# Optimization experiments

Hardware: AMD Instinct MI355X
Metric: run time of the kernel (lower is better)

Reference implementation:

```python
import jax, jax.numpy as jnp
import numpy as np
from jax import lax

V, D, B, S = 50000, 300, 32, 128
H = 1024          # LSTM hidden per direction
NT = 9            # number of CRF tags
BN_EPS = 1e-5


def setup_inputs() -> dict:
    key = jax.random.key(0)
    ks = iter(jax.random.split(key, 48))
    def nrm(shape, scale=0.05):
        return jax.random.normal(next(ks), shape, dtype=jnp.float32) * scale
    inp = {}
    inp["x"] = jax.random.randint(next(ks), (B, S), 0, V)
    inp["y"] = jax.random.randint(next(ks), (B, S), 0, NT)
    inp["mask"] = jnp.ones((B, S), dtype=bool)
    inp["emb"] = nrm((V, D), 0.1)
    inp["lin1_w"] = nrm((512, D)); inp["lin1_b"] = jnp.zeros((512,), jnp.float32)
    in_sizes = [512, 2 * H, 2 * H, 2 * H]
    for l, isz in enumerate(in_sizes):
        inp[f"wih{l}"] = nrm((2, 4 * H, isz))   # [dir, 4H, in]
        inp[f"whh{l}"] = nrm((2, 4 * H, H))
        inp[f"bias{l}"] = jnp.zeros((2, 4 * H), jnp.float32)  # b_ih + b_hh combined
    inp["bn_gamma"] = jnp.ones((2 * H,), jnp.float32)
    inp["bn_beta"] = jnp.zeros((2 * H,), jnp.float32)
    inp["lin2_w"] = nrm((NT, 2 * H)); inp["lin2_b"] = jnp.zeros((NT,), jnp.float32)
    inp["crf_start"] = nrm((NT,), 0.1)
    inp["crf_end"] = nrm((NT,), 0.1)
    inp["crf_trans"] = nrm((NT, NT), 0.1)
    return inp


def _lstm_dir(xs, Wih, Whh, b):
    # xs: [S, B, in] -> hs: [S, B, H]; torch gate order i, f, g, o
    pre = jnp.einsum('sbi,gi->sbg', xs, Wih) + b  # [S,B,4H]
    h0 = jnp.zeros((xs.shape[1], Whh.shape[1]), xs.dtype)
    def step(carry, p):
        h, c = carry
        g = p + h @ Whh.T
        i, f, gg, o = jnp.split(g, 4, axis=-1)
        c = jax.nn.sigmoid(f) * c + jax.nn.sigmoid(i) * jnp.tanh(gg)
        h = jax.nn.sigmoid(o) * jnp.tanh(c)
        return (h, c), h
    _, hs = lax.scan(step, (h0, h0), pre)
    return hs


def _bilstm(xs, Wih, Whh, b):
    fwd = _lstm_dir(xs, Wih[0], Whh[0], b[0])
    bwd = _lstm_dir(xs[::-1], Wih[1], Whh[1], b[1])[::-1]
    return jnp.concatenate([fwd, bwd], axis=-1)


def _crf_llh(emis, tags, mask, start, end, trans):
    # torchcrf CRF forward, batch_first, reduction='sum'
    mf = mask.astype(emis.dtype)
    e_tag = jnp.take_along_axis(emis, tags[..., None], -1)[..., 0]  # [B,S]
    num = start[tags[:, 0]] + e_tag[:, 0]
    tr = trans[tags[:, :-1], tags[:, 1:]]                           # [B,S-1]
    num = num + jnp.sum(mf[:, 1:] * (tr + e_tag[:, 1:]), axis=1)
    lengths = mask.sum(axis=1).astype(jnp.int32)
    last_tag = jnp.take_along_axis(tags, (lengths - 1)[:, None], 1)[:, 0]
    num = num + end[last_tag]
    # forward algorithm (log-sum-exp recurrence over seq)
    alpha0 = start + emis[:, 0]                                     # [B,NT]
    seq_e = jnp.transpose(emis[:, 1:], (1, 0, 2))                   # [S-1,B,NT]
    seq_m = jnp.transpose(mask[:, 1:], (1, 0))                      # [S-1,B]
    def step(alpha, inp):
        e_t, m_t = inp
        nxt = jax.nn.logsumexp(alpha[:, :, None] + trans[None] + e_t[:, None, :], axis=1)
        return jnp.where(m_t[:, None], nxt, alpha), None
    alpha, _ = lax.scan(step, alpha0, (seq_e, seq_m))
    den = jax.nn.logsumexp(alpha + end, axis=1)
    return jnp.sum(num - den)


def reference(x, y, mask, emb, lin1_w, lin1_b,
              wih0, whh0, bias0, wih1, whh1, bias1,
              wih2, whh2, bias2, wih3, whh3, bias3,
              bn_gamma, bn_beta, lin2_w, lin2_b,
              crf_start, crf_end, crf_trans):
    h = emb[x]                          # [B,S,D]
    h = h @ lin1_w.T + lin1_b           # [B,S,512]
    hs = jnp.transpose(h, (1, 0, 2))    # [S,B,512]
    for Wih, Whh, bb in ((wih0, whh0, bias0), (wih1, whh1, bias1),
                         (wih2, whh2, bias2), (wih3, whh3, bias3)):
        hs = _bilstm(hs, Wih, Whh, bb)  # [S,B,2048]
    h = jnp.transpose(hs, (1, 0, 2))    # [B,S,2048]
    # BatchNorm1d eval (running mean 0, var 1) -> affine; ReLU; Dropout eval = id
    h = jax.nn.relu(bn_gamma * h / jnp.sqrt(jnp.float32(1.0 + BN_EPS)) + bn_beta)
    emis = h @ lin2_w.T + lin2_b        # [B,S,9]
    return _crf_llh(emis, y, mask, crf_start, crf_end, crf_trans)
```

## Files before the change

### kernel.cpp

```cpp
#include <hip/hip_runtime.h>
#include <hip/hip_bf16.h>

typedef __attribute__((ext_vector_type(8))) short short8;
typedef __attribute__((ext_vector_type(4))) float f32x4;
typedef unsigned short ushort_t;
typedef unsigned long long u64_t;

__device__ __forceinline__ ushort_t f2bf(float f) {
    __hip_bfloat16 h = __float2bfloat16(f);
    return *(ushort_t*)&h;
}
__device__ __forceinline__ float bf2f(ushort_t u) {
    union { float f; unsigned u32; } x; x.u32 = ((unsigned)u) << 16; return x.f;
}
__device__ __forceinline__ float sigmoidf_(float x) { return 1.0f / (1.0f + expf(-x)); }

__device__ __forceinline__ short8 cvt8(const float* p) {
    short8 r;
    #pragma unroll
    for (int j = 0; j < 8; j++) r[j] = (short)f2bf(p[j]);
    return r;
}

__global__ void lin1_pad(const float* __restrict__ w, ushort_t* __restrict__ d) {
    int idx = blockIdx.x * 256 + threadIdx.x;
    if (idx >= 512 * 320) return;
    int n = idx / 320, k = idx % 320;
    d[idx] = (k < 300) ? f2bf(w[n * 300 + k]) : (ushort_t)0;
}

__global__ void wcvt(const float* __restrict__ w, ushort_t* __restrict__ d, int n) {
    int idx = (blockIdx.x * 256 + threadIdx.x) * 8;
    if (idx >= n) return;
    float tmp[8];
    *(float4*)&tmp[0] = *(const float4*)(w + idx);
    *(float4*)&tmp[4] = *(const float4*)(w + idx + 4);
    *(short8*)&d[idx] = cvt8(tmp);
}

__global__ void emb_gather(const int* __restrict__ x, const float* __restrict__ emb,
                           ushort_t* __restrict__ XE) {
    int tok = blockIdx.x;
    int s = tok >> 5, b = tok & 31;
    int row = x[b * 128 + s];
    const float* e = emb + (size_t)row * 300;
    for (int d = threadIdx.x; d < 320; d += 64)
        XE[(size_t)tok * 320 + d] = (d < 300) ? f2bf(e[d]) : (ushort_t)0;
}

template<bool WF32, bool F32OUT>
__global__ __launch_bounds__(256) void gemm_bias(
    const ushort_t* __restrict__ X, const void* __restrict__ Wv,
    const float* __restrict__ bias, void* __restrict__ Cv,
    int K, int ldx, int ldw, int ldc)
{
    __shared__ __align__(16) ushort_t As[4 * 64 * 8];
    __shared__ __align__(16) ushort_t Bs[4 * 64 * 8];
    const int tid = threadIdx.x;
    const int lane = tid & 63;
    const int w = tid >> 6;
    const int wm = w & 1, wn = w >> 1;
    const int m0 = blockIdx.x * 64, n0 = blockIdx.y * 64;
    const int mt = tid >> 6;
    const int r = lane & 15, q = lane >> 4;
    const ushort_t* xsrc = X + (size_t)(m0 + mt * 16 + r) * ldx + q * 8;
    const ushort_t* wsrcb = WF32 ? nullptr : (const ushort_t*)Wv + (size_t)(n0 + mt * 16 + r) * ldw + q * 8;
    const float*    wsrcf = WF32 ? (const float*)Wv + (size_t)(n0 + mt * 16 + r) * ldw + q * 8 : nullptr;
    f32x4 acc00 = {0,0,0,0}, acc01 = {0,0,0,0}, acc10 = {0,0,0,0}, acc11 = {0,0,0,0};
    for (int k0 = 0; k0 < K; k0 += 32) {
        __syncthreads();
        *(uint4*)&As[(mt * 64 + lane) * 8] = *(const uint4*)(xsrc + k0);
        if (WF32) {
            float tmp[8];
            *(float4*)&tmp[0] = *(const float4*)(wsrcf + k0);
            *(float4*)&tmp[4] = *(const float4*)(wsrcf + k0 + 4);
            *(short8*)&Bs[(mt * 64 + lane) * 8] = cvt8(tmp);
        } else {
            *(uint4*)&Bs[(mt * 64 + lane) * 8] = *(const uint4*)(wsrcb + k0);
        }
        __syncthreads();
        short8 a0 = *(const short8*)&As[((2 * wm    ) * 64 + lane) * 8];
        short8 a1 = *(const short8*)&As[((2 * wm + 1) * 64 + lane) * 8];
        short8 b0 = *(const short8*)&Bs[((2 * wn    ) * 64 + lane) * 8];
        short8 b1 = *(const short8*)&Bs[((2 * wn + 1) * 64 + lane) * 8];
        acc00 = __builtin_amdgcn_mfma_f32_16x16x32_bf16(a0, b0, acc00, 0, 0, 0);
        acc01 = __builtin_amdgcn_mfma_f32_16x16x32_bf16(a0, b1, acc01, 0, 0, 0);
        acc10 = __builtin_amdgcn_mfma_f32_16x16x32_bf16(a1, b0, acc10, 0, 0, 0);
        acc11 = __builtin_amdgcn_mfma_f32_16x16x32_bf16(a1, b1, acc11, 0, 0, 0);
    }
    const int mb = m0 + wm * 32, nb = n0 + wn * 32;
    f32x4 accs[2][2] = {{acc00, acc01}, {acc10, acc11}};
    for (int i = 0; i < 2; i++)
        for (int j = 0; j < 2; j++) {
            int n = nb + j * 16 + r;
            float bv = bias[n];
            #pragma unroll
            for (int reg = 0; reg < 4; reg++) {
                int m = mb + i * 16 + q * 4 + reg;
                float v = accs[i][j][reg] + bv;
                if (F32OUT) ((float*)Cv)[(size_t)m * ldc + n] = v;
                else ((ushort_t*)Cv)[(size_t)m * ldc + n] = f2bf(v);
            }
        }
}

__device__ __forceinline__ void gbar(unsigned* flags, int dir, int slice, int epoch) {
    __syncthreads();
    if (threadIdx.x == 0)
        __hip_atomic_store(&flags[(dir * 32 + slice) * 16], (unsigned)epoch,
                           __ATOMIC_RELAXED, __HIP_MEMORY_SCOPE_AGENT);
    if (threadIdx.x < 64) {
        const unsigned* f = &flags[(dir * 32 + (threadIdx.x & 31)) * 16];
        int spins = 0;
        while (true) {
            unsigned v = __hip_atomic_load(f, __ATOMIC_RELAXED, __HIP_MEMORY_SCOPE_AGENT);
            if (__all(v >= (unsigned)epoch)) break;
            __builtin_amdgcn_s_sleep(1);
            if (++spins >= 65536) {
                spins = 0;
                v = __hip_atomic_load(f, __ATOMIC_ACQUIRE, __HIP_MEMORY_SCOPE_AGENT);
                if (__all(v >= (unsigned)epoch)) break;
            }
        }
    }
    __syncthreads();
}

__global__ __launch_bounds__(512) void lstm_scan(
    const float* __restrict__ PRE,
    const float* __restrict__ WHH,
    ushort_t* __restrict__ H,
    ushort_t* __restrict__ OUT,
    unsigned* __restrict__ flags,
    int epoch0)
{
    const int tid = threadIdx.x;
    const int lane = tid & 63;
    const int w = tid >> 6;
    const int dir = blockIdx.x >> 5;
    const int slice = blockIdx.x & 31;
    const int u0 = slice * 32;
    __shared__ __align__(16) ushort_t Af[2 * 32 * 64 * 8];
    __shared__ float gl[32 * 132];

    const int colw = w * 16 + (lane & 15);
    short8 bfr[32];
    {
        const int gate = colw >> 5, unit = colw & 31;
        const float* wrow = WHH + ((size_t)(dir * 4096 + gate * 1024 + u0 + unit)) * 1024 + (lane >> 4) * 8;
        #pragma unroll
        for (int kc = 0; kc < 32; kc++) {
            float tmp[8];
            *(float4*)&tmp[0] = *(const float4*)(wrow + kc * 32);
            *(float4*)&tmp[4] = *(const float4*)(wrow + kc * 32 + 4);
            bfr[kc] = cvt8(tmp);
        }
    }
    const int eb = tid >> 4, eu = tid & 15;
    float cst0 = 0.f, cst1 = 0.f;
    if ((eu & 1) == 0) {
        ushort_t* hz = H + (size_t)((0 * 2 + dir) * 32 + eb) * 1024 + u0;
        __hip_atomic_store((unsigned*)(hz + eu),      0u, __ATOMIC_RELAXED, __HIP_MEMORY_SCOPE_AGENT);
        __hip_atomic_store((unsigned*)(hz + 16 + eu), 0u, __ATOMIC_RELAXED, __HIP_MEMORY_SCOPE_AGENT);
    }
    int epoch = epoch0 + 1;
    gbar(flags, dir, slice, epoch);

    for (int t = 0; t < 128; t++) {
        const int s = dir ? (127 - t) : t;
        const int bufr = t & 1, bufw = bufr ^ 1;
        const ushort_t* Hsrc = H + (size_t)((bufr * 2 + dir) * 32) * 1024;
        u64_t tmp[16];
        #pragma unroll
        for (int i = 0; i < 8; i++) {
            int c = tid + i * 512;
            int ln = c & 63;
            int kc = (c >> 6) & 31;
            int mt2 = c >> 11;
            int b = mt2 * 16 + (ln & 15);
            int k = kc * 32 + (ln >> 4) * 8;
            const u64_t* src = (const u64_t*)(Hsrc + (size_t)b * 1024 + k);
            tmp[2 * i]     = __hip_atomic_load(src,     __ATOMIC_RELAXED, __HIP_MEMORY_SCOPE_AGENT);
            tmp[2 * i + 1] = __hip_atomic_load(src + 1, __ATOMIC_RELAXED, __HIP_MEMORY_SCOPE_AGENT);
        }
        float pb[8];
        {
            const float* pp = PRE + ((size_t)(s * 32 + eb)) * 8192 + (size_t)dir * 4096 + u0 + eu;
            #pragma unroll
            for (int g = 0; g < 4; g++) {
                pb[2 * g]     = pp[g * 1024];
                pb[2 * g + 1] = pp[g * 1024 + 16];
            }
        }
        #pragma unroll
        for (int i = 0; i < 8; i++) {
            int c = tid + i * 512;
            *(u64_t*)&Af[(size_t)c * 8]     = tmp[2 * i];
            *(u64_t*)&Af[(size_t)c * 8 + 4] = tmp[2 * i + 1];
        }
        __syncthreads();
        f32x4 acc0 = {0,0,0,0}, acc1 = {0,0,0,0};
        #pragma unroll
        for (int kc = 0; kc < 32; kc++) {
            short8 a0 = *(const short8*)&Af[(size_t)((     kc) * 64 + lane) * 8];
            short8 a1 = *(const short8*)&Af[(size_t)((32 + kc) * 64 + lane) * 8];
            acc0 = __builtin_amdgcn_mfma_f32_16x16x32_bf16(a0, bfr[kc], acc0, 0, 0, 0);
            acc1 = __builtin_amdgcn_mfma_f32_16x16x32_bf16(a1, bfr[kc], acc1, 0, 0, 0);
        }
        const int rowb = (lane >> 4) * 4;
        #pragma unroll
        for (int reg = 0; reg < 4; reg++) {
            gl[(rowb + reg) * 132 + colw]        = acc0[reg];
            gl[(16 + rowb + reg) * 132 + colw]   = acc1[reg];
        }
        __syncthreads();
        {
            float gi0 = gl[eb * 132 +  0 + eu] + pb[0];
            float gi1 = gl[eb * 132 + 16 + eu] + pb[1];
            float gf0 = gl[eb * 132 + 32 + eu] + pb[2];
            float gf1 = gl[eb * 132 + 48 + eu] + pb[3];
            float gg0 = gl[eb * 132 + 64 + eu] + pb[4];
            float gg1 = gl[eb * 132 + 80 + eu] + pb[5];
            float go0 = gl[eb * 132 + 96 + eu] + pb[6];
            float go1 = gl[eb * 132 + 112 + eu] + pb[7];
            cst0 = sigmoidf_(gf0) * cst0 + sigmoidf_(gi0) * tanhf(gg0);
            cst1 = sigmoidf_(gf1) * cst1 + sigmoidf_(gi1) * tanhf(gg1);
            float h0 = sigmoidf_(go0) * tanhf(cst0);
            float h1 = sigmoidf_(go1) * tanhf(cst1);
            ushort_t hb0 = f2bf(h0), hb1 = f2bf(h1);
            unsigned o0 = (unsigned)(ushort_t)__shfl_xor((int)(unsigned)hb0, 1);
            unsigned o1 = (unsigned)(ushort_t)__shfl_xor((int)(unsigned)hb1, 1);
            if ((eu & 1) == 0) {
                ushort_t* hw = H + (size_t)((bufw * 2 + dir) * 32 + eb) * 1024 + u0;
                __hip_atomic_store((unsigned*)(hw + eu),      (unsigned)hb0 | (o0 << 16),
                                   __ATOMIC_RELAXED, __HIP_MEMORY_SCOPE_AGENT);
                __hip_atomic_store((unsigned*)(hw + 16 + eu), (unsigned)hb1 | (o1 << 16),
                                   __ATOMIC_RELAXED, __HIP_MEMORY_SCOPE_AGENT);
            }
            ushort_t* op = OUT + ((size_t)(s * 32 + eb)) * 2048 + (size_t)dir * 1024 + u0;
            op[eu] = hb0;
            op[16 + eu] = hb1;
        }
        epoch++;
        gbar(flags, dir, slice, epoch);
    }
}

__global__ __launch_bounds__(256) void emis_kernel(
    const ushort_t* __restrict__ Xf,
    const float* __restrict__ gamma, const float* __restrict__ beta,
    const float* __restrict__ w2, const float* __restrict__ b2,
    float* __restrict__ EM)
{
    const int lane = threadIdx.x & 63;
    const int wv = threadIdx.x >> 6;
    const int tok = blockIdx.x * 4 + wv;
    const int s = tok >> 5, b = tok & 31;
    const float inv = 0.9999950000374997f;
    const int j0 = lane * 4;
    float hn[32];
    #pragma unroll
    for (int c = 0; c < 8; c++) {
        int j = j0 + c * 256;
        u64_t xv = *(const u64_t*)(Xf + (size_t)tok * 2048 + j);
        float4 gv = *(const float4*)(gamma + j);
        float4 bv = *(const float4*)(beta + j);
        float x0 = bf2f((ushort_t)(xv      )), x1 = bf2f((ushort_t)(xv >> 16));
        float x2 = bf2f((ushort_t)(xv >> 32)), x3 = bf2f((ushort_t)(xv >> 48));
        float h0 = gv.x * x0 * inv + bv.x;
        float h1 = gv.y * x1 * inv + bv.y;
        float h2 = gv.z * x2 * inv + bv.z;
        float h3 = gv.w * x3 * inv + bv.w;
        hn[c * 4 + 0] = h0 > 0.f ? h0 : 0.f;
        hn[c * 4 + 1] = h1 > 0.f ? h1 : 0.f;
        hn[c * 4 + 2] = h2 > 0.f ? h2 : 0.f;
        hn[c * 4 + 3] = h3 > 0.f ? h3 : 0.f;
    }
    float acc[9];
    #pragma unroll
    for (int k = 0; k < 9; k++) {
        const float* wr = w2 + (size_t)k * 2048 + j0;
        float a = 0.f;
        #pragma unroll
        for (int c = 0; c < 8; c++) {
            float4 wv4 = *(const float4*)(wr + c * 256);
            a += hn[c * 4 + 0] * wv4.x + hn[c * 4 + 1] * wv4.y
               + hn[c * 4 + 2] * wv4.z + hn[c * 4 + 3] * wv4.w;
        }
        acc[k] = a;
    }
    #pragma unroll
    for (int k = 0; k < 9; k++) {
        #pragma unroll
        for (int off = 32; off > 0; off >>= 1)
            acc[k] += __shfl_xor(acc[k], off);
    }
    if (lane == 0) {
        float* em = EM + ((size_t)b * 128 + s) * 9;
        #pragma unroll
        for (int k = 0; k < 9; k++) em[k] = acc[k] + b2[k];
    }
}

__global__ __launch_bounds__(512) void crf_kernel(
    const float* __restrict__ EM,
    const int* __restrict__ y,
    const float* __restrict__ start, const float* __restrict__ endw,
    const float* __restrict__ trans,
    float* __restrict__ out)
{
    __shared__ float tr[81], st[9], en[9];
    __shared__ float alpha[2][32][12];
    __shared__ float numsh[32], densh[32];
    int tid = threadIdx.x;
    if (tid < 81) tr[tid] = trans[tid];
    if (tid < 9) { st[tid] = start[tid]; en[tid] = endw[tid]; }
    __syncthreads();
    if (tid < 32) {
        int b = tid;
        const int* yb = y + b * 128;
        const float* ebm = EM + (size_t)b * 1152;
        float num = st[yb[0]] + ebm[yb[0]];
        for (int s = 1; s < 128; s++)
            num += tr[yb[s - 1] * 9 + yb[s]] + ebm[s * 9 + yb[s]];
        num += en[yb[127]];
        numsh[b] = num;
    }
    int b = tid / 9, k = tid % 9;
    bool act = tid < 288;
    if (act) alpha[0][b][k] = st[k] + EM[(size_t)b * 1152 + k];
    __syncthreads();
    for (int s = 1; s < 128; s++) {
        int cur = s & 1, prv = cur ^ 1;
        if (act) {
            float m = -1e30f;
            #pragma unroll
            for (int j = 0; j < 9; j++)
                m = fmaxf(m, alpha[prv][b][j] + tr[j * 9 + k]);
            float sum = 0.f;
            #pragma unroll
            for (int j = 0; j < 9; j++)
                sum += expf(alpha[prv][b][j] + tr[j * 9 + k] - m);
            alpha[cur][b][k] = m + logf(sum) + EM[(size_t)b * 1152 + s * 9 + k];
        }
        __syncthreads();
    }
    if (tid < 32) {
        float m = -1e30f;
        for (int j = 0; j < 9; j++) m = fmaxf(m, alpha[1][tid][j] + en[j]);
        float sum = 0.f;
        for (int j = 0; j < 9; j++) sum += expf(alpha[1][tid][j] + en[j] - m);
        densh[tid] = m + logf(sum);
    }
    __syncthreads();
    if (tid == 0) {
        float tot = 0.f;
        for (int bb = 0; bb < 32; bb++) tot += numsh[bb] - densh[bb];
        out[0] = tot;
    }
}

extern "C" void kernel_launch(void* const* d_in, const int* in_sizes, int n_in,
                              void* d_out, int out_size, void* d_ws, size_t ws_size,
                              hipStream_t stream) {
    const int*   x       = (const int*)d_in[0];
    const int*   y       = (const int*)d_in[1];
    const float* emb     = (const float*)d_in[3];
    const float* lin1_w  = (const float*)d_in[4];
    const float* lin1_b  = (const float*)d_in[5];
    const float* wih[4]  = {(const float*)d_in[6],  (const float*)d_in[9],
                            (const float*)d_in[12], (const float*)d_in[15]};
    const float* whh[4]  = {(const float*)d_in[7],  (const float*)d_in[10],
                            (const float*)d_in[13], (const float*)d_in[16]};
    const float* biasl[4]= {(const float*)d_in[8],  (const float*)d_in[11],
                            (const float*)d_in[14], (const float*)d_in[17]};
    const float* bn_g    = (const float*)d_in[18];
    const float* bn_b    = (const float*)d_in[19];
    const float* lin2_w  = (const float*)d_in[20];
    const float* lin2_b  = (const float*)d_in[21];
    const float* crf_s   = (const float*)d_in[22];
    const float* crf_e   = (const float*)d_in[23];
    const float* crf_t   = (const float*)d_in[24];

    char* ws = (char*)d_ws;
    size_t off = 0;
    auto alloc = [&](size_t bytes) { size_t r = off; off += (bytes + 255) & ~(size_t)255; return r; };
    size_t oFLG  = alloc(4096);
    size_t oXE   = alloc((size_t)4096 * 320 * 2);
    size_t oWL1  = alloc((size_t)512 * 320 * 2);
    size_t oXB0  = alloc((size_t)4096 * 2048 * 2);
    size_t oXB1  = alloc((size_t)4096 * 2048 * 2);
    size_t oPRE  = alloc((size_t)4096 * 8192 * 4);
    size_t oH    = alloc((size_t)2 * 2 * 32 * 1024 * 2);
    size_t oEM   = alloc((size_t)32 * 128 * 9 * 4);
    size_t oWB   = alloc((size_t)8192 * 2048 * 2);
    (void)ws_size; (void)in_sizes; (void)n_in; (void)out_size;

    unsigned* flags = (unsigned*)(ws + oFLG);
    ushort_t* XE   = (ushort_t*)(ws + oXE);
    ushort_t* WL1  = (ushort_t*)(ws + oWL1);
    ushort_t* XB0  = (ushort_t*)(ws + oXB0);
    ushort_t* XB1  = (ushort_t*)(ws + oXB1);
    float*    PRE  = (float*)(ws + oPRE);
    ushort_t* Hb   = (ushort_t*)(ws + oH);
    float*    EM   = (float*)(ws + oEM);
    ushort_t* WB   = (ushort_t*)(ws + oWB);

    hipMemsetAsync(ws + oFLG, 0, 4096, stream);
    emb_gather<<<4096, 64, 0, stream>>>(x, emb, XE);
    lin1_pad<<<(512 * 320 + 255) / 256, 256, 0, stream>>>(lin1_w, WL1);
    gemm_bias<false, false><<<dim3(64, 8), 256, 0, stream>>>(XE, WL1, lin1_b, XB0, 320, 320, 320, 512);

    for (int l = 0; l < 4; l++) {
        int Kl = (l == 0) ? 512 : 2048;
        ushort_t* Xin  = (l % 2 == 0) ? XB0 : XB1;
        ushort_t* Xout = (l % 2 == 0) ? XB1 : XB0;
        int nw = 8192 * Kl;
        wcvt<<<nw / 2048, 256, 0, stream>>>(wih[l], WB, nw);
        gemm_bias<false, true><<<dim3(64, 128), 256, 0, stream>>>(Xin, WB, biasl[l], PRE,
                                                                  Kl, Kl, Kl, 8192);
        lstm_scan<<<64, 512, 0, stream>>>(PRE, whh[l], Hb, Xout, flags, l * 129);
    }
    emis_kernel<<<1024, 256, 0, stream>>>(XB0, bn_g, bn_b, lin2_w, lin2_b, EM);
    crf_kernel<<<1, 512, 0, stream>>>(EM, y, crf_s, crf_e, crf_t, (float*)d_out);
}
```

Baseline: 5.726 ms.

## Permute input-projection output per slice and prefetch next step's gate inputs

The input-projection GEMM now writes its fp32 output in a layout ordered by direction, slice and timestep, with each thread's two units held next to each other, so the LSTM scan can read its eight gate pre-activations as four float2 loads from one contiguous region. The scan also issues the loads for step t+1 during step t, taking global-memory latency off the serial recurrence. In exchange, the GEMM epilogue does scattered stores and needs more address arithmetic, and the scan holds a few extra registers.

New measurement: 5.682 ms. No clear change (-0.8%).

```diff
diff --git a/kernel.cpp b/kernel.cpp
--- a/kernel.cpp
+++ b/kernel.cpp
@@ -48,7 +48,7 @@
         XE[(size_t)tok * 320 + d] = (d < 300) ? f2bf(e[d]) : (ushort_t)0;
 }
 
-template<bool WF32, bool F32OUT>
+template<bool WF32, bool F32OUT, bool PERM>
 __global__ __launch_bounds__(256) void gemm_bias(
     const ushort_t* __restrict__ X, const void* __restrict__ Wv,
     const float* __restrict__ bias, void* __restrict__ Cv,
@@ -94,12 +94,26 @@
         for (int j = 0; j < 2; j++) {
             int n = nb + j * 16 + r;
             float bv = bias[n];
-            #pragma unroll
-            for (int reg = 0; reg < 4; reg++) {
-                int m = mb + i * 16 + q * 4 + reg;
-                float v = accs[i][j][reg] + bv;
-                if (F32OUT) ((float*)Cv)[(size_t)m * ldc + n] = v;
-                else ((ushort_t*)Cv)[(size_t)m * ldc + n] = f2bf(v);
+            if (PERM) {
+                int dirn = n >> 12, c = n & 4095;
+                int gate = c >> 10, unit = c & 1023;
+                int slice = unit >> 5, ue5 = unit & 31;
+                int pos = ((ue5 & 15) << 1) | (ue5 >> 4);
+                float* base = (float*)Cv + ((size_t)(dirn * 32 + slice) * 128) * 4096 + gate * 32 + pos;
+                #pragma unroll
+                for (int reg = 0; reg < 4; reg++) {
+                    int m = mb + i * 16 + q * 4 + reg;
+                    int ss = m >> 5, bb = m & 31;
+                    base[(size_t)ss * 4096 + bb * 128] = accs[i][j][reg] + bv;
+                }
+            } else {
+                #pragma unroll
+                for (int reg = 0; reg < 4; reg++) {
+                    int m = mb + i * 16 + q * 4 + reg;
+                    float v = accs[i][j][reg] + bv;
+                    if (F32OUT) ((float*)Cv)[(size_t)m * ldc + n] = v;
+                    else ((ushort_t*)Cv)[(size_t)m * ldc + n] = f2bf(v);
+                }
             }
         }
 }
@@ -163,6 +177,15 @@
         __hip_atomic_store((unsigned*)(hz + eu),      0u, __ATOMIC_RELAXED, __HIP_MEMORY_SCOPE_AGENT);
         __hip_atomic_store((unsigned*)(hz + 16 + eu), 0u, __ATOMIC_RELAXED, __HIP_MEMORY_SCOPE_AGENT);
     }
+    const float* pbase = PRE + ((size_t)(dir * 32 + slice) * 128) * 4096 + eb * 128 + (eu << 1);
+    float2 pb0, pb1, pb2, pb3;
+    {
+        const float* pp = pbase + (size_t)(dir ? 127 : 0) * 4096;
+        pb0 = *(const float2*)(pp);
+        pb1 = *(const float2*)(pp + 32);
+        pb2 = *(const float2*)(pp + 64);
+        pb3 = *(const float2*)(pp + 96);
+    }
     int epoch = epoch0 + 1;
     gbar(flags, dir, slice, epoch);
 
@@ -183,15 +206,6 @@
             tmp[2 * i]     = __hip_atomic_load(src,     __ATOMIC_RELAXED, __HIP_MEMORY_SCOPE_AGENT);
             tmp[2 * i + 1] = __hip_atomic_load(src + 1, __ATOMIC_RELAXED, __HIP_MEMORY_SCOPE_AGENT);
         }
-        float pb[8];
-        {
-            const float* pp = PRE + ((size_t)(s * 32 + eb)) * 8192 + (size_t)dir * 4096 + u0 + eu;
-            #pragma unroll
-            for (int g = 0; g < 4; g++) {
-                pb[2 * g]     = pp[g * 1024];
-                pb[2 * g + 1] = pp[g * 1024 + 16];
-            }
-        }
         #pragma unroll
         for (int i = 0; i < 8; i++) {
             int c = tid + i * 512;
@@ -215,14 +229,21 @@
         }
         __syncthreads();
         {
-            float gi0 = gl[eb * 132 +  0 + eu] + pb[0];
-            float gi1 = gl[eb * 132 + 16 + eu] + pb[1];
-            float gf0 = gl[eb * 132 + 32 + eu] + pb[2];
-            float gf1 = gl[eb * 132 + 48 + eu] + pb[3];
-            float gg0 = gl[eb * 132 + 64 + eu] + pb[4];
-            float gg1 = gl[eb * 132 + 80 + eu] + pb[5];
-            float go0 = gl[eb * 132 + 96 + eu] + pb[6];
-            float go1 = gl[eb * 132 + 112 + eu] + pb[7];
+            float gi0 = gl[eb * 132 +   0 + eu] + pb0.x;
+            float gi1 = gl[eb * 132 +  16 + eu] + pb0.y;
+            float gf0 = gl[eb * 132 +  32 + eu] + pb1.x;
+            float gf1 = gl[eb * 132 +  48 + eu] + pb1.y;
+            float gg0 = gl[eb * 132 +  64 + eu] + pb2.x;
+            float gg1 = gl[eb * 132 +  80 + eu] + pb2.y;
+            float go0 = gl[eb * 132 +  96 + eu] + pb3.x;
+            float go1 = gl[eb * 132 + 112 + eu] + pb3.y;
+            if (t < 127) {
+                const float* pp = pbase + (size_t)(dir ? (126 - t) : (t + 1)) * 4096;
+                pb0 = *(const float2*)(pp);
+                pb1 = *(const float2*)(pp + 32);
+                pb2 = *(const float2*)(pp + 64);
+                pb3 = *(const float2*)(pp + 96);
+            }
             cst0 = sigmoidf_(gf0) * cst0 + sigmoidf_(gi0) * tanhf(gg0);
             cst1 = sigmoidf_(gf1) * cst1 + sigmoidf_(gi1) * tanhf(gg1);
             float h0 = sigmoidf_(go0) * tanhf(cst0);
@@ -409,7 +430,7 @@
     hipMemsetAsync(ws + oFLG, 0, 4096, stream);
     emb_gather<<<4096, 64, 0, stream>>>(x, emb, XE);
     lin1_pad<<<(512 * 320 + 255) / 256, 256, 0, stream>>>(lin1_w, WL1);
-    gemm_bias<false, false><<<dim3(64, 8), 256, 0, stream>>>(XE, WL1, lin1_b, XB0, 320, 320, 320, 512);
+    gemm_bias<false, false, false><<<dim3(64, 8), 256, 0, stream>>>(XE, WL1, lin1_b, XB0, 320, 320, 320, 512);
 
     for (int l = 0; l < 4; l++) {
         int Kl = (l == 0) ? 512 : 2048;
@@ -417,8 +438,8 @@
         ushort_t* Xout = (l % 2 == 0) ? XB1 : XB0;
         int nw = 8192 * Kl;
         wcvt<<<nw / 2048, 256, 0, stream>>>(wih[l], WB, nw);
-        gemm_bias<false, true><<<dim3(64, 128), 256, 0, stream>>>(Xin, WB, biasl[l], PRE,
-                                                                  Kl, Kl, Kl, 8192);
+        gemm_bias<false, true, true><<<dim3(64, 128), 256, 0, stream>>>(Xin, WB, biasl[l], PRE,
+                                                                        Kl, Kl, Kl, 8192);
         lstm_scan<<<64, 512, 0, stream>>>(PRE, whh[l], Hb, Xout, flags, l * 129);
     }
     emis_kernel<<<1024, 256, 0, stream>>>(XB0, bn_g, bn_b, lin2_w, lin2_b, EM);
```
